# Performance work log

Hardware: AMD Instinct MI355X
Metric: run time of the kernel (lower is better)

Reference implementation:

```python
import jax, jax.numpy as jnp
import numpy as np

N = 4_000_000

def setup_inputs() -> dict:
    key = jax.random.key(0)
    k1, k2, k3, k4 = jax.random.split(key, 4)
    return {
        "rot_kf": jax.random.normal(k1, (N, 3, 3), dtype=jnp.float32),
        "pose_kf": jax.random.normal(k2, (N, 3), dtype=jnp.float32),
        "rot_gt": jax.random.normal(k3, (N, 3, 3), dtype=jnp.float32),
        "pose_gt": jax.random.normal(k4, (N, 3), dtype=jnp.float32),
    }


def reference(rot_kf, pose_kf, rot_gt, pose_gt):
    # Per frame i: M_kf_inv @ M_gt where M_kf_inv = [R_kf^T, -R_kf^T p_kf; 0 1]
    # => relative rotation R_rel = R_kf^T @ R_gt
    #    relative translation t_rel = R_kf^T @ (p_gt - p_kf)
    # ||relative_se3 - I4||_F^2 = ||R_rel - I3||_F^2 + ||t_rel||^2
    # (bottom row [0,0,0,1] matches identity exactly)
    R_rel = jnp.einsum('nji,njk->nik', rot_kf, rot_gt)          # [N,3,3]
    t_rel = jnp.einsum('nji,nj->ni', rot_kf, pose_gt - pose_kf)  # [N,3]
    eye3 = jnp.eye(3, dtype=R_rel.dtype)
    s_error = jnp.sum((R_rel - eye3) ** 2, axis=(1, 2)) + jnp.sum(t_rel ** 2, axis=1)  # [N]
    return jnp.sqrt(jnp.mean(s_error)) + 1e-8
```

## Files before the change

### kernel.cpp

```cpp
#include <hip/hip_runtime.h>
#include <math.h>

#define BLOCK 256
#define FPC   256
#define F4M   (FPC * 9 / 4)
#define NBLOCKS 2048

__global__ __launch_bounds__(BLOCK, 8) void rmse_partial_kernel(
    const float* __restrict__ rot_kf, const float* __restrict__ pose_kf,
    const float* __restrict__ rot_gt, const float* __restrict__ pose_gt,
    float* __restrict__ partial, int N)
{
    __shared__ float ldsA[FPC * 9];
    __shared__ float ldsB[FPC * 9];
    __shared__ float redbuf[BLOCK / 64];

    const int tid = threadIdx.x;
    const long long totalF4 = (long long)N * 9 / 4;
    const long long totalRotF = (long long)N * 9;
    const int nChunks = (int)(((long long)N + FPC - 1) / FPC);

    float sum = 0.0f;

    for (int c = blockIdx.x; c < nChunks; c += gridDim.x) {
        const long long base4 = (long long)c * F4M;

        __syncthreads();

        for (int i = tid; i < F4M; i += BLOCK) {
            const long long f4 = base4 + i;
            float4 v = make_float4(0.f, 0.f, 0.f, 0.f);
            if (f4 * 4 + 3 < totalRotF) v = reinterpret_cast<const float4*>(rot_kf)[f4];
            reinterpret_cast<float4*>(ldsA)[i] = v;
        }
        for (int i = tid; i < F4M; i += BLOCK) {
            const long long f4 = base4 + i;
            float4 v = make_float4(0.f, 0.f, 0.f, 0.f);
            if (f4 * 4 + 3 < totalRotF) v = reinterpret_cast<const float4*>(rot_gt)[f4];
            reinterpret_cast<float4*>(ldsB)[i] = v;
        }
        __syncthreads();

        const int f = c * FPC + tid;
        if (f < N) {
            float a[9], b[9];
            #pragma unroll
            for (int j = 0; j < 9; ++j) a[j] = ldsA[tid * 9 + j];
            #pragma unroll
            for (int j = 0; j < 9; ++j) b[j] = ldsB[tid * 9 + j];

            const long long p = (long long)f * 3;
            const float d0 = pose_gt[p + 0] - pose_kf[p + 0];
            const float d1 = pose_gt[p + 1] - pose_kf[p + 1];
            const float d2 = pose_gt[p + 2] - pose_kf[p + 2];

            float se = 0.0f;
            #pragma unroll
            for (int i = 0; i < 3; ++i) {
                #pragma unroll
                for (int k = 0; k < 3; ++k) {
                    float r = a[i] * b[k] + a[3 + i] * b[3 + k] + a[6 + i] * b[6 + k];
                    r -= (i == k) ? 1.0f : 0.0f;
                    se += r * r;
                }
                const float t = a[i] * d0 + a[3 + i] * d1 + a[6 + i] * d2;
                se += t * t;
            }
            sum += se;
        }
    }

    const int lane = tid & 63;
    const int wave = tid >> 6;
    #pragma unroll
    for (int off = 32; off > 0; off >>= 1) sum += __shfl_down(sum, off);
    if (lane == 0) redbuf[wave] = sum;
    __syncthreads();
    if (tid == 0) {
        float s = 0.0f;
        #pragma unroll
        for (int w = 0; w < BLOCK / 64; ++w) s += redbuf[w];
        partial[blockIdx.x] = s;
    }
}

__global__ __launch_bounds__(BLOCK) void rmse_finalize_kernel(
    const float* __restrict__ partial, int nPartial, float* __restrict__ out, int N)
{
    __shared__ float redbuf[BLOCK / 64];
    float sum = 0.0f;
    for (int i = threadIdx.x; i < nPartial; i += BLOCK) sum += partial[i];
    #pragma unroll
    for (int off = 32; off > 0; off >>= 1) sum += __shfl_down(sum, off);
    const int lane = threadIdx.x & 63;
    const int wave = threadIdx.x >> 6;
    if (lane == 0) redbuf[wave] = sum;
    __syncthreads();
    if (threadIdx.x == 0) {
        float s = 0.0f;
        #pragma unroll
        for (int w = 0; w < BLOCK / 64; ++w) s += redbuf[w];
        out[0] = sqrtf(s / (float)N) + 1e-8f;
    }
}

extern "C" void kernel_launch(void* const* d_in, const int* in_sizes, int n_in,
                              void* d_out, int out_size, void* d_ws, size_t ws_size,
                              hipStream_t stream) {
    const float* rot_kf  = (const float*)d_in[0];
    const float* pose_kf = (const float*)d_in[1];
    const float* rot_gt  = (const float*)d_in[2];
    const float* pose_gt = (const float*)d_in[3];
    float* out = (float*)d_out;
    float* partial = (float*)d_ws;

    const int N = in_sizes[1] / 3;
    const int nChunks = (int)(((long long)N + FPC - 1) / FPC);

    int grid = NBLOCKS;
    if (grid > nChunks) grid = nChunks;
    const int wsCap = (int)(ws_size / sizeof(float));
    if (grid > wsCap) grid = wsCap;
    if (grid < 1) grid = 1;

    rmse_partial_kernel<<<grid, BLOCK, 0, stream>>>(rot_kf, pose_kf, rot_gt, pose_gt, partial, N);
    rmse_finalize_kernel<<<1, BLOCK, 0, stream>>>(partial, grid, out, N);
}
```

Before: 69.25 us.

## Use direct global-to-LDS loads and atomic work-stealing chunk scheduling

Rotation tiles are now copied straight from global memory into LDS with the global_load_lds builtin, so the data no longer passes through registers. Out-of-range float4 indices are clamped instead of zero-filled. Blocks now take chunks from a global atomic counter instead of a fixed grid-stride schedule, aiming to balance load across CUs. This adds a hipMemsetAsync before each launch and per-chunk atomics and barriers. Clamped tail loads rely on the f<N guard to avoid counting garbage data.

```diff
diff --git a/kernel.cpp b/kernel.cpp
--- a/kernel.cpp
+++ b/kernel.cpp
@@ -6,39 +6,48 @@
 #define F4M   (FPC * 9 / 4)
 #define NBLOCKS 2048
 
+#define GLOAD_LDS16(gp, lp)                                                     \
+  __builtin_amdgcn_global_load_lds(                                             \
+      (const __attribute__((address_space(1))) void*)(gp),                      \
+      (__attribute__((address_space(3))) void*)(lp), 16, 0, 0)
+
 __global__ __launch_bounds__(BLOCK, 8) void rmse_partial_kernel(
     const float* __restrict__ rot_kf, const float* __restrict__ pose_kf,
     const float* __restrict__ rot_gt, const float* __restrict__ pose_gt,
-    float* __restrict__ partial, int N)
+    int* __restrict__ counter, float* __restrict__ partial, int N)
 {
     __shared__ float ldsA[FPC * 9];
     __shared__ float ldsB[FPC * 9];
     __shared__ float redbuf[BLOCK / 64];
+    __shared__ int   nextc;
 
     const int tid = threadIdx.x;
-    const long long totalF4 = (long long)N * 9 / 4;
     const long long totalRotF = (long long)N * 9;
+    const long long rotF4max = (totalRotF >= 4) ? (totalRotF - 4) / 4 : 0;
     const int nChunks = (int)(((long long)N + FPC - 1) / FPC);
 
     float sum = 0.0f;
 
-    for (int c = blockIdx.x; c < nChunks; c += gridDim.x) {
+    if (tid == 0) nextc = atomicAdd(counter, 1);
+    __syncthreads();
+    int c = nextc;
+
+    while (c < nChunks) {
         const long long base4 = (long long)c * F4M;
 
-        __syncthreads();
-
         for (int i = tid; i < F4M; i += BLOCK) {
-            const long long f4 = base4 + i;
-            float4 v = make_float4(0.f, 0.f, 0.f, 0.f);
-            if (f4 * 4 + 3 < totalRotF) v = reinterpret_cast<const float4*>(rot_kf)[f4];
-            reinterpret_cast<float4*>(ldsA)[i] = v;
+            long long f4 = base4 + i;
+            if (f4 > rotF4max) f4 = rotF4max;
+            GLOAD_LDS16(reinterpret_cast<const float4*>(rot_kf) + f4,
+                        (void*)(reinterpret_cast<float4*>(ldsA) + i));
         }
         for (int i = tid; i < F4M; i += BLOCK) {
-            const long long f4 = base4 + i;
-            float4 v = make_float4(0.f, 0.f, 0.f, 0.f);
-            if (f4 * 4 + 3 < totalRotF) v = reinterpret_cast<const float4*>(rot_gt)[f4];
-            reinterpret_cast<float4*>(ldsB)[i] = v;
+            long long f4 = base4 + i;
+            if (f4 > rotF4max) f4 = rotF4max;
+            GLOAD_LDS16(reinterpret_cast<const float4*>(rot_gt) + f4,
+                        (void*)(reinterpret_cast<float4*>(ldsB) + i));
         }
+        if (tid == 0) nextc = atomicAdd(counter, 1);
         __syncthreads();
 
         const int f = c * FPC + tid;
@@ -68,6 +77,10 @@
             }
             sum += se;
         }
+
+        const int cn = nextc;
+        __syncthreads();
+        c = cn;
     }
 
     const int lane = tid & 63;
@@ -112,17 +125,21 @@
     const float* rot_gt  = (const float*)d_in[2];
     const float* pose_gt = (const float*)d_in[3];
     float* out = (float*)d_out;
-    float* partial = (float*)d_ws;
+
+    int*   counter = (int*)d_ws;
+    float* partial = (float*)((char*)d_ws + 256);
 
     const int N = in_sizes[1] / 3;
     const int nChunks = (int)(((long long)N + FPC - 1) / FPC);
 
     int grid = NBLOCKS;
     if (grid > nChunks) grid = nChunks;
-    const int wsCap = (int)(ws_size / sizeof(float));
+    const int wsCap = (int)((ws_size - 256) / sizeof(float));
     if (grid > wsCap) grid = wsCap;
     if (grid < 1) grid = 1;
 
-    rmse_partial_kernel<<<grid, BLOCK, 0, stream>>>(rot_kf, pose_kf, rot_gt, pose_gt, partial, N);
+    hipMemsetAsync(counter, 0, sizeof(int), stream);
+    rmse_partial_kernel<<<grid, BLOCK, 0, stream>>>(rot_kf, pose_kf, rot_gt, pose_gt,
+                                                    counter, partial, N);
     rmse_finalize_kernel<<<1, BLOCK, 0, stream>>>(partial, grid, out, N);
 }
```

Measured after the change: 222.6 us. +221.4%, slower.
